# Performance work log

Hardware: AMD Instinct MI355X
Metric: run time of the kernel (lower is better)

## Reference

```python
import jax, jax.numpy as jnp
import numpy as np

N = 10000      # nodes
E = 160000     # directed edges (script symmetrizes; random here)
IN = 512       # input feature dim
H = 512        # hidden dim
OUT = 16       # classes


def setup_inputs() -> dict:
    key = jax.random.key(0)
    ks = jax.random.split(key, 8)
    x = jax.random.normal(ks[0], (N, IN), dtype=jnp.float32)
    edge_index = jax.random.randint(ks[1], (2, E), 0, N, dtype=jnp.int64)

    def glorot(k, shape):
        lim = np.sqrt(6.0 / (shape[0] + shape[1])).astype(np.float32)
        return jax.random.uniform(k, shape, dtype=jnp.float32, minval=-lim, maxval=lim)

    W1 = glorot(ks[2], (IN, H));  b1 = jnp.zeros((H,), jnp.float32)
    W2 = glorot(ks[3], (H, H));   b2 = jnp.zeros((H,), jnp.float32)
    Wl = glorot(ks[4], (H, OUT)); bl = jnp.zeros((OUT,), jnp.float32)
    return {"x": x, "edge_index": edge_index,
            "W1": W1, "b1": b1, "W2": W2, "b2": b2, "Wl": Wl, "bl": bl}


def gcn_conv(x, edge_index, W, b):
    """PyG GCNConv: D^{-1/2}(A+I)D^{-1/2} X W + b, unit edge weights."""
    n = x.shape[0]
    src, dst = edge_index[0], edge_index[1]
    h = x @ W                                   # [N, H] transform first (in<=out path)
    # degree with self-loops (all edge weights = 1)
    deg = jnp.zeros((n,), h.dtype).at[dst].add(1.0) + 1.0
    dinv = jax.lax.rsqrt(deg)                   # deg >= 1, no inf handling needed
    norm = dinv[src] * dinv[dst]                # [E]
    msgs = norm[:, None] * h[src]               # [E, H] gather + scale
    agg = jax.ops.segment_sum(msgs, dst, num_segments=n)
    agg = agg + (dinv * dinv)[:, None] * h      # self-loop contribution
    return agg + b


def reference(x, edge_index, W1, b1, W2, b2, Wl, bl):
    h = jax.nn.relu(gcn_conv(x, edge_index, W1, b1))
    # dropout is identity at inference
    h = jax.nn.relu(gcn_conv(h, edge_index, W2, b2))
    return h @ Wl + bl                          # [N, OUT] logits
```

## Files before the change

kernel.cpp:

```cpp
#include <hip/hip_runtime.h>
#include <stdint.h>

#define NF 512
#define OUT_F 16
#define PAD_DEG 64
#define GBM 64
#define GBN 128

typedef __attribute__((ext_vector_type(8))) _Float16 half8;
typedef __attribute__((ext_vector_type(4))) _Float16 half4v;
typedef __attribute__((ext_vector_type(4))) float f32x4;

#define GLOAD_LDS16(g, l) \
  __builtin_amdgcn_global_load_lds((const __attribute__((address_space(1))) unsigned int*)(g), \
                                   (__attribute__((address_space(3))) unsigned int*)(l), 16, 0, 0)


__global__ __launch_bounds__(256) void prep_kernel(
    const float* __restrict__ W1, const float* __restrict__ W2,
    _Float16* __restrict__ T1, _Float16* __restrict__ T2,
    const float* __restrict__ x, _Float16* __restrict__ x16,
    const int* __restrict__ src, const int* __restrict__ dst,
    int* __restrict__ counts, int* __restrict__ src_pad,
    int E, int Nreal, int Mp) {
    __shared__ float tile[64][65];
    int b = blockIdx.x;
    int xblocks = Mp / 4;

    if (b < 128) {
        int id = b;
        const float* W;  _Float16* WT;
        if (id < 64) { W = W1; WT = T1; }
        else         { W = W2; WT = T2; id -= 64; }
        int k0 = (id & 7) * 64, n0 = (id >> 3) * 64;
        int tr = threadIdx.x >> 4;
        int tc4 = (threadIdx.x & 15) * 4;
#pragma unroll
        for (int i = 0; i < 4; ++i) {
            int r = tr + i * 16;
            float4 v = *(const float4*)(W + (size_t)(k0 + r) * NF + n0 + tc4);
            tile[r][tc4 + 0] = v.x; tile[r][tc4 + 1] = v.y;
            tile[r][tc4 + 2] = v.z; tile[r][tc4 + 3] = v.w;
        }
        __syncthreads();
#pragma unroll
        for (int i = 0; i < 4; ++i) {
            int n = tr + i * 16;
            half4v hv;
#pragma unroll
            for (int j = 0; j < 4; ++j) hv[j] = (_Float16)tile[tc4 + j][n];
            *(half4v*)(WT + (size_t)(n0 + n) * NF + k0 + tc4) = hv;
        }
    } else if (b < 128 + xblocks) {
        int idx = (b - 128) * 256 + threadIdx.x;
        int row = idx >> 6;
        int c8 = (idx & 63) * 8;
        if (row >= Mp) return;
        half8 hv = {0, 0, 0, 0, 0, 0, 0, 0};
        if (row < Nreal) {
            float4 v0 = *(const float4*)(x + (size_t)row * NF + c8);
            float4 v1 = *(const float4*)(x + (size_t)row * NF + c8 + 4);
            hv[0] = (_Float16)v0.x; hv[1] = (_Float16)v0.y;
            hv[2] = (_Float16)v0.z; hv[3] = (_Float16)v0.w;
            hv[4] = (_Float16)v1.x; hv[5] = (_Float16)v1.y;
            hv[6] = (_Float16)v1.z; hv[7] = (_Float16)v1.w;
        }
        *(half8*)(x16 + (size_t)row * NF + c8) = hv;
    } else {
        int e = (b - 128 - xblocks) * 256 + threadIdx.x;
        if (e < E) {
            int d = dst[e];
            int slot = atomicAdd(&counts[d], 1);
            if (slot < PAD_DEG) src_pad[(size_t)d * PAD_DEG + slot] = src[e];
        }
    }
}


__global__ __launch_bounds__(256) void gemm_mfma_kernel(
    const _Float16* __restrict__ A, const _Float16* __restrict__ BT,
    const int* __restrict__ counts, _Float16* __restrict__ Ch, int nstripes) {
    __shared__ _Float16 lds[GBM * 64 + GBN * 64];
    _Float16* As = lds;
    _Float16* Bs = lds + GBM * 64;

    int b = blockIdx.x;
    int xcd = b & 7;
    int r = b >> 3;
    int s = xcd + 8 * (r >> 2);
    if (s >= nstripes) return;
    int m0 = s * GBM;
    int n0 = (r & 3) * GBN;

    int t = threadIdx.x;
    int w = t >> 6, lane = t & 63, l15 = lane & 15, q = lane >> 4;
    int wr = w >> 1, wc = w & 1;

    int gr = lane >> 3;
    int gc = ((lane & 7) ^ (gr & 7)) * 8;
    const _Float16* Ag0 = A + (size_t)(m0 + w * 8 + gr) * NF + gc;
    const _Float16* Ag1 = A + (size_t)(m0 + 32 + w * 8 + gr) * NF + gc;
    const _Float16* Bg0 = BT + (size_t)(n0 + w * 8 + gr) * NF + gc;
    const _Float16* Bg1 = BT + (size_t)(n0 + 32 + w * 8 + gr) * NF + gc;
    const _Float16* Bg2 = BT + (size_t)(n0 + 64 + w * 8 + gr) * NF + gc;
    const _Float16* Bg3 = BT + (size_t)(n0 + 96 + w * 8 + gr) * NF + gc;
    _Float16* As_d0 = As + (w * 8) * 64;
    _Float16* As_d1 = As + (32 + w * 8) * 64;
    _Float16* Bs_d0 = Bs + (w * 8) * 64;
    _Float16* Bs_d1 = Bs + (32 + w * 8) * 64;
    _Float16* Bs_d2 = Bs + (64 + w * 8) * 64;
    _Float16* Bs_d3 = Bs + (96 + w * 8) * 64;

    f32x4 acc[2][4] = {};

    for (int k0 = 0; k0 < NF; k0 += 64) {
        GLOAD_LDS16(Ag0 + k0, As_d0);
        GLOAD_LDS16(Ag1 + k0, As_d1);
        GLOAD_LDS16(Bg0 + k0, Bs_d0);
        GLOAD_LDS16(Bg1 + k0, Bs_d1);
        GLOAD_LDS16(Bg2 + k0, Bs_d2);
        GLOAD_LDS16(Bg3 + k0, Bs_d3);
        __syncthreads();

        int key = l15 & 7;
#pragma unroll
        for (int kk = 0; kk < 2; ++kk) {
            int ch = ((kk * 4 + q) ^ key) * 8;
            half8 a[2], b2[4];
#pragma unroll
            for (int rr = 0; rr < 2; ++rr)
                a[rr] = *(const half8*)(As + (wr * 32 + rr * 16 + l15) * 64 + ch);
#pragma unroll
            for (int c = 0; c < 4; ++c)
                b2[c] = *(const half8*)(Bs + (wc * 64 + c * 16 + l15) * 64 + ch);
#pragma unroll
            for (int rr = 0; rr < 2; ++rr)
#pragma unroll
                for (int c = 0; c < 4; ++c)
                    acc[rr][c] = __builtin_amdgcn_mfma_f32_16x16x32_f16(a[rr], b2[c], acc[rr][c], 0, 0, 0);
        }
        __syncthreads();
    }

#pragma unroll
    for (int rr = 0; rr < 2; ++rr)
#pragma unroll
        for (int i = 0; i < 4; ++i) {
            int row = m0 + wr * 32 + rr * 16 + q * 4 + i;
            float dv = rsqrtf((float)counts[row] + 1.0f);
#pragma unroll
            for (int c = 0; c < 4; ++c) {
                int col = n0 + wc * 64 + c * 16 + l15;
                Ch[(size_t)row * NF + col] = (_Float16)(acc[rr][c][i] * dv);
            }
        }
}


__global__ __launch_bounds__(256) void agg_kernel(
    const _Float16* __restrict__ hb, const int* __restrict__ counts,
    const int* __restrict__ src_pad, const float* __restrict__ bias,
    _Float16* __restrict__ out_h, int Mreal) {
    int node = __builtin_amdgcn_readfirstlane(blockIdx.x * 4 + (threadIdx.x >> 6));
    int lane = threadIdx.x & 63;
    int f8 = lane * 8;
    size_t obase = (size_t)node * NF + f8;

    if (node >= Mreal) {
        half8 z = {0, 0, 0, 0, 0, 0, 0, 0};
        *(half8*)(out_h + obase) = z;
        return;
    }

    int cntr = counts[node];
    int cnt = cntr < PAD_DEG ? cntr : PAD_DEG;
    const int* sp = src_pad + (size_t)node * PAD_DEG;

    half8 sv = *(const half8*)(hb + obase);
    float4 b0 = *(const float4*)(bias + f8);
    float4 b1 = *(const float4*)(bias + f8 + 4);

    float acc[8] = {};
    int e = 0;
    for (; e + 7 < cnt; e += 8) {
        half8 v[8];
#pragma unroll
        for (int u = 0; u < 8; ++u) {
            int s = sp[e + u];
            v[u] = *(const half8*)(hb + (size_t)s * NF + f8);
        }
#pragma unroll
        for (int k = 0; k < 8; ++k)
            acc[k] += (((float)v[0][k] + (float)v[1][k]) + ((float)v[2][k] + (float)v[3][k]))
                    + (((float)v[4][k] + (float)v[5][k]) + ((float)v[6][k] + (float)v[7][k]));
    }
    for (; e + 3 < cnt; e += 4) {
        int s0 = sp[e], s1 = sp[e + 1], s2 = sp[e + 2], s3 = sp[e + 3];
        half8 v0 = *(const half8*)(hb + (size_t)s0 * NF + f8);
        half8 v1 = *(const half8*)(hb + (size_t)s1 * NF + f8);
        half8 v2 = *(const half8*)(hb + (size_t)s2 * NF + f8);
        half8 v3 = *(const half8*)(hb + (size_t)s3 * NF + f8);
#pragma unroll
        for (int k = 0; k < 8; ++k)
            acc[k] += ((float)v0[k] + (float)v1[k]) + ((float)v2[k] + (float)v3[k]);
    }
    for (; e < cnt; ++e) {
        int s = sp[e];
        half8 v = *(const half8*)(hb + (size_t)s * NF + f8);
#pragma unroll
        for (int k = 0; k < 8; ++k) acc[k] += (float)v[k];
    }

    float dv = rsqrtf((float)cntr + 1.0f);
    float bb[8] = {b0.x, b0.y, b0.z, b0.w, b1.x, b1.y, b1.z, b1.w};
    half8 o8;
#pragma unroll
    for (int k = 0; k < 8; ++k) {
        float o = fmaxf(fmaf(dv, acc[k] + (float)sv[k], bb[k]), 0.f);
        o8[k] = (_Float16)o;
    }
    *(half8*)(out_h + obase) = o8;
}


__global__ __launch_bounds__(256) void head_kernel(
    const _Float16* __restrict__ in, const float* __restrict__ Wl,
    const float* __restrict__ bl, float* __restrict__ out, int M) {
    __shared__ float Ws[NF * OUT_F];
    int tid = threadIdx.x;
    for (int i = tid; i < NF * OUT_F; i += 256) Ws[i] = Wl[i];
    __syncthreads();
    int node = blockIdx.x * 16 + (tid >> 4);
    int o = tid & 15;
    if (node >= M) return;
    const half8* row8 = (const half8*)(in + (size_t)node * NF);
    float acc = 0.f;
#pragma unroll 2
    for (int k8 = 0; k8 < NF / 8; ++k8) {
        half8 hv = row8[k8];
        int kb = k8 * 8;
#pragma unroll
        for (int u = 0; u < 8; ++u)
            acc = fmaf((float)hv[u], Ws[(kb + u) * OUT_F + o], acc);
    }
    out[(size_t)node * OUT_F + o] = acc + bl[o];
}


extern "C" void kernel_launch(void* const* d_in, const int* in_sizes, int n_in,
                              void* d_out, int out_size, void* d_ws, size_t ws_size,
                              hipStream_t stream) {
    const float* x  = (const float*)d_in[0];
    const int* eidx = (const int*)d_in[1];
    const float* W1 = (const float*)d_in[2];
    const float* b1 = (const float*)d_in[3];
    const float* W2 = (const float*)d_in[4];
    const float* b2 = (const float*)d_in[5];
    const float* Wl = (const float*)d_in[6];
    const float* bl = (const float*)d_in[7];

    int N = in_sizes[0] / NF;
    int E = in_sizes[1] / 2;
    int Mp = (N + GBM - 1) & ~(GBM - 1);
    const int* src = eidx;
    const int* dst = eidx + E;

    char* p = (char*)d_ws;
    auto carve = [&](size_t bytes) -> void* {
        void* r = (void*)p;
        p += (bytes + 255) & ~(size_t)255;
        return r;
    };
    _Float16* hbuf = (_Float16*)carve((size_t)Mp * NF * sizeof(_Float16));
    _Float16* abuf = (_Float16*)carve((size_t)Mp * NF * sizeof(_Float16));
    _Float16* W1T  = (_Float16*)carve((size_t)NF * NF * sizeof(_Float16));
    _Float16* W2T  = (_Float16*)carve((size_t)NF * NF * sizeof(_Float16));
    int* counts    = (int*)carve((size_t)Mp * sizeof(int));
    int* src_pad   = (int*)carve((size_t)N * PAD_DEG * sizeof(int));

    hipMemsetAsync(counts, 0, (size_t)Mp * sizeof(int), stream);

    int xblocks = Mp / 4;
    int eblocks = (E + 255) / 256;
    prep_kernel<<<dim3(128 + xblocks + eblocks), dim3(256), 0, stream>>>(
        W1, W2, W1T, W2T, x, abuf, src, dst, counts, src_pad, E, N, Mp);

    int nstripes = Mp / GBM;
    int spx = (nstripes + 7) / 8;
    dim3 gg(8 * spx * 4);
    dim3 ga(Mp / 4);

    gemm_mfma_kernel<<<gg, dim3(256), 0, stream>>>(abuf, W1T, counts, hbuf, nstripes);
    agg_kernel<<<ga, dim3(256), 0, stream>>>(hbuf, counts, src_pad, b1, abuf, N);
    gemm_mfma_kernel<<<gg, dim3(256), 0, stream>>>(abuf, W2T, counts, hbuf, nstripes);
    agg_kernel<<<ga, dim3(256), 0, stream>>>(hbuf, counts, src_pad, b2, abuf, N);
    head_kernel<<<dim3((N + 15) / 16), dim3(256), 0, stream>>>(abuf, Wl, bl, (float*)d_out, N);
}
```

Measured before the change: 167.8 us.

## Double-buffer GEMM LDS, narrow source indices to u16, split aggregation by feature slice

The GEMM kernel now uses two LDS buffers so the next K tile's global-to-LDS loads are issued while the current tile is computed, hiding load latency at the cost of doubled shared memory. The padded neighbour index table is stored as 16-bit values instead of 32-bit, halving index traffic. This relies on node ids fitting in 16 bits, which holds for N=10000. The aggregation kernel is restructured so each block handles a 64-column slice with 8 edges in flight per wave, reduced through cross-lane shuffles. That trades more blocks and shuffle work for more memory-level parallelism and better locality per slice.

```diff
diff --git a/kernel.cpp b/kernel.cpp
--- a/kernel.cpp
+++ b/kernel.cpp
@@ -21,7 +21,7 @@
     _Float16* __restrict__ T1, _Float16* __restrict__ T2,
     const float* __restrict__ x, _Float16* __restrict__ x16,
     const int* __restrict__ src, const int* __restrict__ dst,
-    int* __restrict__ counts, int* __restrict__ src_pad,
+    int* __restrict__ counts, unsigned short* __restrict__ src_pad,
     int E, int Nreal, int Mp) {
     __shared__ float tile[64][65];
     int b = blockIdx.x;
@@ -71,7 +71,7 @@
         if (e < E) {
             int d = dst[e];
             int slot = atomicAdd(&counts[d], 1);
-            if (slot < PAD_DEG) src_pad[(size_t)d * PAD_DEG + slot] = src[e];
+            if (slot < PAD_DEG) src_pad[(size_t)d * PAD_DEG + slot] = (unsigned short)src[e];
         }
     }
 }
@@ -80,9 +80,11 @@
 __global__ __launch_bounds__(256) void gemm_mfma_kernel(
     const _Float16* __restrict__ A, const _Float16* __restrict__ BT,
     const int* __restrict__ counts, _Float16* __restrict__ Ch, int nstripes) {
-    __shared__ _Float16 lds[GBM * 64 + GBN * 64];
-    _Float16* As = lds;
-    _Float16* Bs = lds + GBM * 64;
+    __shared__ _Float16 lds[2 * (GBM * 64 + GBN * 64)];
+    _Float16* As0 = lds;
+    _Float16* Bs0 = lds + GBM * 64;
+    _Float16* As1 = lds + (GBM * 64 + GBN * 64);
+    _Float16* Bs1 = As1 + GBM * 64;
 
     int b = blockIdx.x;
     int xcd = b & 7;
@@ -104,42 +106,47 @@
     const _Float16* Bg1 = BT + (size_t)(n0 + 32 + w * 8 + gr) * NF + gc;
     const _Float16* Bg2 = BT + (size_t)(n0 + 64 + w * 8 + gr) * NF + gc;
     const _Float16* Bg3 = BT + (size_t)(n0 + 96 + w * 8 + gr) * NF + gc;
-    _Float16* As_d0 = As + (w * 8) * 64;
-    _Float16* As_d1 = As + (32 + w * 8) * 64;
-    _Float16* Bs_d0 = Bs + (w * 8) * 64;
-    _Float16* Bs_d1 = Bs + (32 + w * 8) * 64;
-    _Float16* Bs_d2 = Bs + (64 + w * 8) * 64;
-    _Float16* Bs_d3 = Bs + (96 + w * 8) * 64;
 
     f32x4 acc[2][4] = {};
 
-    for (int k0 = 0; k0 < NF; k0 += 64) {
-        GLOAD_LDS16(Ag0 + k0, As_d0);
-        GLOAD_LDS16(Ag1 + k0, As_d1);
-        GLOAD_LDS16(Bg0 + k0, Bs_d0);
-        GLOAD_LDS16(Bg1 + k0, Bs_d1);
-        GLOAD_LDS16(Bg2 + k0, Bs_d2);
-        GLOAD_LDS16(Bg3 + k0, Bs_d3);
-        __syncthreads();
-
+    auto stage = [&](_Float16* Asb, _Float16* Bsb, int k0) {
+        GLOAD_LDS16(Ag0 + k0, Asb + (w * 8) * 64);
+        GLOAD_LDS16(Ag1 + k0, Asb + (32 + w * 8) * 64);
+        GLOAD_LDS16(Bg0 + k0, Bsb + (w * 8) * 64);
+        GLOAD_LDS16(Bg1 + k0, Bsb + (32 + w * 8) * 64);
+        GLOAD_LDS16(Bg2 + k0, Bsb + (64 + w * 8) * 64);
+        GLOAD_LDS16(Bg3 + k0, Bsb + (96 + w * 8) * 64);
+    };
+
+    auto compute = [&](const _Float16* Asb, const _Float16* Bsb) {
         int key = l15 & 7;
 #pragma unroll
         for (int kk = 0; kk < 2; ++kk) {
             int ch = ((kk * 4 + q) ^ key) * 8;
-            half8 a[2], b2[4];
+            half8 a[2], bv[4];
 #pragma unroll
             for (int rr = 0; rr < 2; ++rr)
-                a[rr] = *(const half8*)(As + (wr * 32 + rr * 16 + l15) * 64 + ch);
+                a[rr] = *(const half8*)(Asb + (wr * 32 + rr * 16 + l15) * 64 + ch);
 #pragma unroll
             for (int c = 0; c < 4; ++c)
-                b2[c] = *(const half8*)(Bs + (wc * 64 + c * 16 + l15) * 64 + ch);
+                bv[c] = *(const half8*)(Bsb + (wc * 64 + c * 16 + l15) * 64 + ch);
 #pragma unroll
             for (int rr = 0; rr < 2; ++rr)
 #pragma unroll
                 for (int c = 0; c < 4; ++c)
-                    acc[rr][c] = __builtin_amdgcn_mfma_f32_16x16x32_f16(a[rr], b2[c], acc[rr][c], 0, 0, 0);
-        }
+                    acc[rr][c] = __builtin_amdgcn_mfma_f32_16x16x32_f16(a[rr], bv[c], acc[rr][c], 0, 0, 0);
+        }
+    };
+
+    stage(As0, Bs0, 0);
+#pragma unroll
+    for (int kt = 0; kt < NF / 64; kt += 2) {
         __syncthreads();
+        if (kt + 1 < NF / 64) stage(As1, Bs1, (kt + 1) * 64);
+        compute(As0, Bs0);
+        __syncthreads();
+        if (kt + 2 < NF / 64) stage(As0, Bs0, (kt + 2) * 64);
+        compute(As1, Bs1);
     }
 
 #pragma unroll
@@ -159,67 +166,67 @@
 
 __global__ __launch_bounds__(256) void agg_kernel(
     const _Float16* __restrict__ hb, const int* __restrict__ counts,
-    const int* __restrict__ src_pad, const float* __restrict__ bias,
+    const unsigned short* __restrict__ src_pad, const float* __restrict__ bias,
     _Float16* __restrict__ out_h, int Mreal) {
-    int node = __builtin_amdgcn_readfirstlane(blockIdx.x * 4 + (threadIdx.x >> 6));
-    int lane = threadIdx.x & 63;
-    int f8 = lane * 8;
-    size_t obase = (size_t)node * NF + f8;
+    int b = blockIdx.x;
+    int slice = b & 7;
+    int grp = b >> 3;
+    int w = threadIdx.x >> 6, lane = threadIdx.x & 63;
+    int node = __builtin_amdgcn_readfirstlane(grp * 4 + w);
+    int e8 = lane >> 3, f8 = lane & 7;
+    int col = slice * 64 + f8 * 8;
 
     if (node >= Mreal) {
-        half8 z = {0, 0, 0, 0, 0, 0, 0, 0};
-        *(half8*)(out_h + obase) = z;
+        if (lane < 8) {
+            half8 z = {0, 0, 0, 0, 0, 0, 0, 0};
+            *(half8*)(out_h + (size_t)node * NF + col) = z;
+        }
         return;
     }
 
     int cntr = counts[node];
     int cnt = cntr < PAD_DEG ? cntr : PAD_DEG;
-    const int* sp = src_pad + (size_t)node * PAD_DEG;
-
-    half8 sv = *(const half8*)(hb + obase);
-    float4 b0 = *(const float4*)(bias + f8);
-    float4 b1 = *(const float4*)(bias + f8 + 4);
+    const unsigned short* sp = src_pad + (size_t)node * PAD_DEG;
 
     float acc[8] = {};
-    int e = 0;
-    for (; e + 7 < cnt; e += 8) {
-        half8 v[8];
-#pragma unroll
-        for (int u = 0; u < 8; ++u) {
-            int s = sp[e + u];
-            v[u] = *(const half8*)(hb + (size_t)s * NF + f8);
-        }
+    for (int e = 0; e < cnt; e += 16) {
+        half8 v0 = {0, 0, 0, 0, 0, 0, 0, 0};
+        half8 v1 = {0, 0, 0, 0, 0, 0, 0, 0};
+        int i0 = e + e8, i1 = i0 + 8;
+        if (i0 < cnt) {
+            int s0 = sp[i0];
+            v0 = *(const half8*)(hb + (size_t)s0 * NF + col);
+        }
+        if (i1 < cnt) {
+            int s1 = sp[i1];
+            v1 = *(const half8*)(hb + (size_t)s1 * NF + col);
+        }
+#pragma unroll
+        for (int k = 0; k < 8; ++k) acc[k] += (float)v0[k] + (float)v1[k];
+    }
+
+    if (e8 == 0) {
+        half8 sv = *(const half8*)(hb + (size_t)node * NF + col);
+#pragma unroll
+        for (int k = 0; k < 8; ++k) acc[k] += (float)sv[k];
+    }
+
+#pragma unroll
+    for (int m = 8; m <= 32; m <<= 1)
+#pragma unroll
+        for (int k = 0; k < 8; ++k) acc[k] += __shfl_xor(acc[k], m, 64);
+
+    if (lane < 8) {
+        float dv = rsqrtf((float)cntr + 1.0f);
+        float4 b0 = *(const float4*)(bias + col);
+        float4 b1v = *(const float4*)(bias + col + 4);
+        float bb[8] = {b0.x, b0.y, b0.z, b0.w, b1v.x, b1v.y, b1v.z, b1v.w};
+        half8 o8;
 #pragma unroll
         for (int k = 0; k < 8; ++k)
-            acc[k] += (((float)v[0][k] + (float)v[1][k]) + ((float)v[2][k] + (float)v[3][k]))
-                    + (((float)v[4][k] + (float)v[5][k]) + ((float)v[6][k] + (float)v[7][k]));
-    }
-    for (; e + 3 < cnt; e += 4) {
-        int s0 = sp[e], s1 = sp[e + 1], s2 = sp[e + 2], s3 = sp[e + 3];
-        half8 v0 = *(const half8*)(hb + (size_t)s0 * NF + f8);
-        half8 v1 = *(const half8*)(hb + (size_t)s1 * NF + f8);
-        half8 v2 = *(const half8*)(hb + (size_t)s2 * NF + f8);
-        half8 v3 = *(const half8*)(hb + (size_t)s3 * NF + f8);
-#pragma unroll
-        for (int k = 0; k < 8; ++k)
-            acc[k] += ((float)v0[k] + (float)v1[k]) + ((float)v2[k] + (float)v3[k]);
-    }
-    for (; e < cnt; ++e) {
-        int s = sp[e];
-        half8 v = *(const half8*)(hb + (size_t)s * NF + f8);
-#pragma unroll
-        for (int k = 0; k < 8; ++k) acc[k] += (float)v[k];
-    }
-
-    float dv = rsqrtf((float)cntr + 1.0f);
-    float bb[8] = {b0.x, b0.y, b0.z, b0.w, b1.x, b1.y, b1.z, b1.w};
-    half8 o8;
-#pragma unroll
-    for (int k = 0; k < 8; ++k) {
-        float o = fmaxf(fmaf(dv, acc[k] + (float)sv[k], bb[k]), 0.f);
-        o8[k] = (_Float16)o;
-    }
-    *(half8*)(out_h + obase) = o8;
+            o8[k] = (_Float16)fmaxf(fmaf(dv, acc[k], bb[k]), 0.f);
+        *(half8*)(out_h + (size_t)node * NF + col) = o8;
+    }
 }
 
 
@@ -276,7 +283,7 @@
     _Float16* W1T  = (_Float16*)carve((size_t)NF * NF * sizeof(_Float16));
     _Float16* W2T  = (_Float16*)carve((size_t)NF * NF * sizeof(_Float16));
     int* counts    = (int*)carve((size_t)Mp * sizeof(int));
-    int* src_pad   = (int*)carve((size_t)N * PAD_DEG * sizeof(int));
+    unsigned short* src_pad = (unsigned short*)carve((size_t)N * PAD_DEG * sizeof(unsigned short));
 
     hipMemsetAsync(counts, 0, (size_t)Mp * sizeof(int), stream);
 
@@ -288,7 +295,7 @@
     int nstripes = Mp / GBM;
     int spx = (nstripes + 7) / 8;
     dim3 gg(8 * spx * 4);
-    dim3 ga(Mp / 4);
+    dim3 ga(8 * (Mp / 4));
 
     gemm_mfma_kernel<<<gg, dim3(256), 0, stream>>>(abuf, W1T, counts, hbuf, nstripes);
     agg_kernel<<<ga, dim3(256), 0, stream>>>(hbuf, counts, src_pad, b1, abuf, N);
```

After: 187.8 us. 11.9% more time.
